# Kernel tuning notes

Hardware: AMD Instinct MI355X
Metric: run time of the kernel (lower is better)

The kernel has to match this reference:

```python
import jax, jax.numpy as jnp
import numpy as np

B, T, E, H, V = 64, 512, 512, 512, 50000

def setup_inputs() -> dict:
    key = jax.random.key(0)
    ks = jax.random.split(key, 8)
    x = jax.random.randint(ks[0], (B, T), 0, V)
    h0 = jax.random.normal(ks[1], (B, H), jnp.float32) * 0.1
    c0 = jax.random.normal(ks[2], (B, H), jnp.float32) * 0.1
    emb = jax.random.normal(ks[3], (V, E), jnp.float32) * 0.02
    emb = emb.at[0].set(0.0)  # padding_idx=0
    s_i = 1.0 / np.sqrt(H)
    W_ih = jax.random.uniform(ks[4], (4 * H, E), jnp.float32, -s_i, s_i)
    W_hh = jax.random.uniform(ks[5], (4 * H, H), jnp.float32, -s_i, s_i)
    b_ih = jax.random.uniform(ks[6], (4 * H,), jnp.float32, -s_i, s_i)
    b_hh = jax.random.uniform(ks[7], (4 * H,), jnp.float32, -s_i, s_i)
    return {"x": x, "h0": h0, "c0": c0, "emb": emb,
            "W_ih": W_ih, "W_hh": W_hh, "b_ih": b_ih, "b_hh": b_hh}

def reference(x, h0, c0, emb, W_ih, W_hh, b_ih, b_hh):
    # embedding lookup (option 'a'): [B, T, E]
    xs = emb[x]
    # precompute input-to-gate projections for all timesteps: [B, T, 4H]
    pre = jnp.einsum('bte,ge->btg', xs, W_ih) + b_ih + b_hh
    pre_t = jnp.swapaxes(pre, 0, 1)  # [T, B, 4H]

    def step(carry, p_t):
        h, c = carry
        gates = p_t + h @ W_hh.T  # [B, 4H]
        i, f, g, o = jnp.split(gates, 4, axis=-1)
        i = jax.nn.sigmoid(i)
        f = jax.nn.sigmoid(f)
        g = jnp.tanh(g)
        o = jax.nn.sigmoid(o)
        c_new = f * c + i * g
        h_new = o * jnp.tanh(c_new)
        return (h_new, c_new), h_new

    _, hs = jax.lax.scan(step, (h0, c0), pre_t)  # hs: [T, B, H]
    # original stacks per-batch lists of per-timestep hidden states -> [B, T, H]
    return jnp.swapaxes(hs, 0, 1)
```

## Files before the change

### kernel.cpp

```cpp
#include <hip/hip_runtime.h>
#include <stdint.h>

typedef __attribute__((ext_vector_type(8))) short short8;
typedef __attribute__((ext_vector_type(4))) short short4_;
typedef __attribute__((ext_vector_type(4))) float f4;
typedef __attribute__((ext_vector_type(4))) uint32_t u32x4;

#define B_ 64
#define T_ 512
#define E_ 512
#define H_ 512
#define GH 2048

static __device__ __forceinline__ uint16_t f2bf(float f) {
  uint32_t u = __builtin_bit_cast(uint32_t, f);
  uint32_t r = (u + 0x7FFFu + ((u >> 16) & 1u)) >> 16;
  return (uint16_t)r;
}
static __device__ __forceinline__ float bf2f(uint16_t b) {
  return __builtin_bit_cast(float, (uint32_t)b << 16);
}
static __device__ __forceinline__ float sigmoidf_(float x) {
  return 1.0f / (1.0f + __expf(-x));
}
static __device__ __forceinline__ float tanhf_(float x) {
  float e = __expf(-2.0f * fabsf(x));
  float t = (1.0f - e) / (1.0f + e);
  return __builtin_copysignf(t, x);
}

static __device__ __forceinline__ u32x4 ld_flag4_cc(const int* p) {
  u32x4 v;
  asm volatile("global_load_dwordx4 %0, %1, off sc0 sc1\n\ts_waitcnt vmcnt(0)"
               : "=v"(v) : "v"(p) : "memory");
  return v;
}
static __device__ __forceinline__ void ld_x4_cc(u32x4* d, const void* p) {
  asm volatile("global_load_dwordx4 %0, %1, off sc0 sc1" : "=v"(*d) : "v"(p));
}
static __device__ __forceinline__ void st_u32_cc(uint32_t* p, uint32_t v) {
  asm volatile("global_store_dword %0, %1, off sc0 sc1" :: "v"(p), "v"(v) : "memory");
}
static __device__ __forceinline__ void st_flag_cc(int* p, int v) {
  asm volatile("global_store_dword %0, %1, off sc0 sc1" :: "v"(p), "v"(v) : "memory");
}

__global__ void k_prep(const float* __restrict__ Whh, uint16_t* __restrict__ Whi_g,
                       uint16_t* __restrict__ Wlo_g) {
  int i = blockIdx.x * 256 + threadIdx.x;
  float w = Whh[i];
  uint16_t hi = f2bf(w);
  Whi_g[i] = hi;
  Wlo_g[i] = f2bf(w - bf2f(hi));
}

__global__ void k_init(const float* __restrict__ h0, uint32_t* __restrict__ hP0,
                       int* __restrict__ flags) {
  int i = blockIdx.x * 256 + threadIdx.x;
  if (i < B_ * H_) {
    float v = h0[i];
    uint16_t hi = f2bf(v);
    uint16_t lo = f2bf(v - bf2f(hi));
    hP0[i] = (uint32_t)hi | ((uint32_t)lo << 16);
  }
  if (i < 128) flags[i] = 0;
}

__launch_bounds__(256)
__global__ void k_pre(const int* __restrict__ x, const float* __restrict__ emb,
                      const float* __restrict__ Wih, const float* __restrict__ bih,
                      const float* __restrict__ bhh, float* __restrict__ pre2, int t0) {
  __shared__ uint16_t As[128 * 64];
  __shared__ uint16_t Bs[128 * 64];
  const int tid = threadIdx.x;
  const int tm = blockIdx.x >> 4;
  const int tn = blockIdx.x & 15;
  const int wid = tid >> 6, lane = tid & 63;
  const int wr = wid >> 1, wc = wid & 1;

  const int arow = tid >> 1;
  const int half = tid & 1;
  const int m = tm * 128 + arow;
  const int bb = m & 63;
  const int tt = t0 + (m >> 6);
  const int xid = x[bb * T_ + tt];
  const float* asrc = emb + (size_t)xid * E_ + half * 32;
  const float* bsrc = Wih + (size_t)(tn * 128 + arow) * E_ + half * 32;

  f4 acc[4][4];
#pragma unroll
  for (int a = 0; a < 4; ++a)
#pragma unroll
    for (int b = 0; b < 4; ++b) acc[a][b] = (f4){0.f, 0.f, 0.f, 0.f};

  for (int kk = 0; kk < 8; ++kk) {
    __syncthreads();
#pragma unroll
    for (int gi = 0; gi < 4; ++gi) {
      f4 a0 = *(const f4*)(asrc + kk * 64 + gi * 8);
      f4 a1 = *(const f4*)(asrc + kk * 64 + gi * 8 + 4);
      f4 b0 = *(const f4*)(bsrc + kk * 64 + gi * 8);
      f4 b1 = *(const f4*)(bsrc + kk * 64 + gi * 8 + 4);
      short8 va, vb;
#pragma unroll
      for (int j = 0; j < 4; ++j) {
        va[j] = (short)f2bf(a0[j]); va[4 + j] = (short)f2bf(a1[j]);
        vb[j] = (short)f2bf(b0[j]); vb[4 + j] = (short)f2bf(b1[j]);
      }
      int kq = half * 4 + gi;
      *(short8*)(As + arow * 64 + (kq ^ (arow & 7)) * 8) = va;
      *(short8*)(Bs + arow * 64 + (kq ^ (arow & 7)) * 8) = vb;
    }
    __syncthreads();
#pragma unroll
    for (int ks = 0; ks < 2; ++ks) {
      short8 af[4], bfr[4];
#pragma unroll
      for (int mi = 0; mi < 4; ++mi) {
        int row = wr * 64 + mi * 16 + (lane & 15);
        int kq = ks * 4 + (lane >> 4);
        af[mi] = *(const short8*)(As + row * 64 + (kq ^ (row & 7)) * 8);
      }
#pragma unroll
      for (int ni = 0; ni < 4; ++ni) {
        int row = wc * 64 + ni * 16 + (lane & 15);
        int kq = ks * 4 + (lane >> 4);
        bfr[ni] = *(const short8*)(Bs + row * 64 + (kq ^ (row & 7)) * 8);
      }
#pragma unroll
      for (int mi = 0; mi < 4; ++mi)
#pragma unroll
        for (int ni = 0; ni < 4; ++ni)
          acc[mi][ni] = __builtin_amdgcn_mfma_f32_16x16x32_bf16(af[mi], bfr[ni], acc[mi][ni], 0, 0, 0);
    }
  }
#pragma unroll
  for (int ni = 0; ni < 4; ++ni) {
    int n = tn * 128 + wc * 64 + ni * 16 + (lane & 15);
    float bias = bih[n] + bhh[n];
    int q = n >> 9, u = n & 511;
    int ug = u >> 4, uloc = u & 15;
    int gl = q * 16 + uloc;
#pragma unroll
    for (int mi = 0; mi < 4; ++mi) {
      int mrow = tm * 128 + wr * 64 + mi * 16 + (lane >> 4) * 4;
      int trel = mrow >> 6;
      int bbr = mrow & 63;
      f4 vst;
#pragma unroll
      for (int j = 0; j < 4; ++j) vst[j] = acc[mi][ni][j] + bias;
      float* dst = pre2 + (((size_t)trel * 32 + ug) * 4 + (bbr >> 4)) * 1024 + gl * 16 + (bbr & 15);
      __builtin_nontemporal_store(vst, (f4*)dst);
    }
  }
}

__launch_bounds__(256)
__global__ void k_lstm(const float* __restrict__ pre2, const uint16_t* __restrict__ Whi_g,
                       const uint16_t* __restrict__ Wlo_g, const float* __restrict__ c0,
                       float* __restrict__ out, uint32_t* __restrict__ hP0,
                       uint32_t* __restrict__ hP1, float* __restrict__ c_state,
                       int* __restrict__ flags, int t0, int TB) {
  extern __shared__ char smem[];
  uint16_t* WhiL = (uint16_t*)smem;
  uint16_t* WloL = (uint16_t*)(smem + 65536);
  uint16_t* Hh   = (uint16_t*)(smem + 131072);
  uint16_t* Hl   = (uint16_t*)(smem + 147456);

  const int tid = threadIdx.x;
  const int bg = blockIdx.x & 3;
  const int ug = blockIdx.x >> 2;
  const int wv = tid >> 6, lane = tid & 63;
  const int wi = lane & 15, hi4 = lane >> 4;
  const int q = wi & 3, v = wi >> 2;
  const int u = ug * 16 + wv * 4 + v;
  const int gl = q * 16 + wv * 4 + v;

  for (int it = 0; it < 16; ++it) {
    int gg = it * 256 + tid;
    int r = gg >> 6, kq = gg & 63;
    int grow = (r & 3) * 512 + ug * 16 + (r >> 4) * 4 + ((r >> 2) & 3);
    short8 whi = *(const short8*)(Whi_g + (size_t)grow * 512 + kq * 8);
    short8 wlo = *(const short8*)(Wlo_g + (size_t)grow * 512 + kq * 8);
    int kqs = (kq & ~7) | ((kq & 7) ^ (r & 7));
    *(short8*)(WhiL + r * 512 + kqs * 8) = whi;
    *(short8*)(WloL + r * 512 + kqs * 8) = wlo;
  }

  f4 c_reg;
  {
    const float* csrc = (t0 == 0) ? c0 : c_state;
    const int brow = bg * 16 + hi4 * 4;
#pragma unroll
    for (int j = 0; j < 4; ++j) c_reg[j] = csrc[(size_t)(brow + j) * H_ + u];
  }
  int* fbase = flags + bg * 32;
  int* myflag = fbase + ug;
  u32x4 fv0 = (u32x4){0, 0, 0, 0};
  float hq_prev = 0.0f;
  const int rowloc = hi4 * 4 + q;
  const int b = bg * 16 + rowloc;
  __syncthreads();

  for (int s = t0 + 1; s <= t0 + TB; ++s) {
    const uint32_t* hsrc = (((s - 1) & 1) ? hP1 : hP0) + (size_t)bg * 16 * 512;
    uint32_t* hdst = ((s & 1) ? hP1 : hP0) + (size_t)bg * 16 * 512;

    f4 accA, accB, accC;
    {
      const f4* pp = (const f4*)(pre2 + (((size_t)(s - 1 - t0) * 32 + ug) * 4 + bg) * 1024 +
                                 gl * 16 + hi4 * 4);
      accA = __builtin_nontemporal_load(pp);
      accB = (f4){0.f, 0.f, 0.f, 0.f};
      accC = accB;
    }

    {
      const int target = s - 1;
      bool ok = true;
      if (lane < 8)
        ok = (int)fv0[0] >= target && (int)fv0[1] >= target &&
             (int)fv0[2] >= target && (int)fv0[3] >= target;
      int guard = 0;
      while (!__all(ok)) {
        __builtin_amdgcn_s_sleep(1);
        ok = true;
        if (lane < 8) {
          u32x4 fv = ld_flag4_cc(fbase + lane * 4);
          ok = (int)fv[0] >= target && (int)fv[1] >= target &&
               (int)fv[2] >= target && (int)fv[3] >= target;
        }
        if (++guard > (1 << 17)) break;
      }
    }

    u32x4 d[8];
#pragma unroll
    for (int jj = 0; jj < 8; ++jj) {
      int local = jj * 64 + lane;
      int row = local >> 5;
      int u0v = wv * 128 + (local & 31) * 4;
      ld_x4_cc(&d[jj], hsrc + (size_t)row * 512 + u0v);
    }
    if (s > t0 + 1) {
      float* optr = out + (size_t)b * (T_ * H_) + (size_t)(s - 2) * H_ + u;
      asm volatile("global_store_dword %0, %1, off" :: "v"(optr), "v"(hq_prev) : "memory");
      asm volatile("s_waitcnt vmcnt(1)" ::: "memory");
    } else {
      asm volatile("s_waitcnt vmcnt(0)" ::: "memory");
    }
    __builtin_amdgcn_sched_barrier(0);
#pragma unroll
    for (int jj = 0; jj < 8; ++jj) asm volatile("" : "+v"(d[jj]));
#pragma unroll
    for (int jj = 0; jj < 8; ++jj) {
      int local = jj * 64 + lane;
      int row = local >> 5;
      int u0v = wv * 128 + (local & 31) * 4;
      int kq = u0v >> 3, half = (u0v >> 2) & 1;
      int kqs = (kq & ~7) | ((kq & 7) ^ (row & 7));
      short4_ hh, hl;
#pragma unroll
      for (int i = 0; i < 4; ++i) {
        hh[i] = (short)(d[jj][i] & 0xFFFFu);
        hl[i] = (short)(d[jj][i] >> 16);
      }
      *(short4_*)(Hh + row * 512 + kqs * 8 + half * 4) = hh;
      *(short4_*)(Hl + row * 512 + kqs * 8 + half * 4) = hl;
    }
    __syncthreads();

    f4 accA2 = (f4){0.f, 0.f, 0.f, 0.f}, accB2 = accA2, accC2 = accA2;
    const int br = wv * 16 + wi;
#pragma unroll
    for (int ks2 = 0; ks2 < 8; ++ks2) {
#pragma unroll
      for (int p = 0; p < 2; ++p) {
        int ks = ks2 * 2 + p;
        int kq = ks * 4 + hi4;
        int kqsA = (kq & ~7) | ((kq & 7) ^ (wi & 7));
        int kqsB = (kq & ~7) | ((kq & 7) ^ (br & 7));
        short8 ah = *(const short8*)(Hh + wi * 512 + kqsA * 8);
        short8 al = *(const short8*)(Hl + wi * 512 + kqsA * 8);
        short8 bh = *(const short8*)(WhiL + br * 512 + kqsB * 8);
        short8 bl = *(const short8*)(WloL + br * 512 + kqsB * 8);
        if (p == 0) {
          accA = __builtin_amdgcn_mfma_f32_16x16x32_bf16(ah, bh, accA, 0, 0, 0);
          accB = __builtin_amdgcn_mfma_f32_16x16x32_bf16(al, bh, accB, 0, 0, 0);
          accC = __builtin_amdgcn_mfma_f32_16x16x32_bf16(ah, bl, accC, 0, 0, 0);
        } else {
          accA2 = __builtin_amdgcn_mfma_f32_16x16x32_bf16(ah, bh, accA2, 0, 0, 0);
          accB2 = __builtin_amdgcn_mfma_f32_16x16x32_bf16(al, bh, accB2, 0, 0, 0);
          accC2 = __builtin_amdgcn_mfma_f32_16x16x32_bf16(ah, bl, accC2, 0, 0, 0);
        }
      }
    }

    const bool qb0 = (q & 1) != 0, qb1 = (q & 2) != 0;
    f4 a0;
#pragma unroll
    for (int j = 0; j < 4; ++j)
      a0[j] = (accA[j] + accA2[j]) + (accB[j] + accB2[j]) + (accC[j] + accC2[j]);
    f4 x1, s1a, s1b, x2a, x2b;
#pragma unroll
    for (int j = 0; j < 4; ++j) x1[j] = __shfl_xor(a0[j], 1);
#pragma unroll
    for (int j = 0; j < 4; ++j) {
      s1a[j] = qb0 ? x1[j] : a0[j];
      s1b[j] = qb0 ? a0[j] : x1[j];
    }
#pragma unroll
    for (int j = 0; j < 4; ++j) {
      x2a[j] = __shfl_xor(s1a[j], 2);
      x2b[j] = __shfl_xor(s1b[j], 2);
    }
    f4 cn, hn;
#pragma unroll
    for (int j = 0; j < 4; ++j) {
      float gi = qb1 ? x2a[j] : s1a[j];
      float gg = qb1 ? s1a[j] : x2a[j];
      float gf = qb1 ? x2b[j] : s1b[j];
      float go = qb1 ? s1b[j] : x2b[j];
      float iv = sigmoidf_(gi);
      float fv = sigmoidf_(gf);
      float gv = tanhf_(gg);
      float ov = sigmoidf_(go);
      float c2 = fv * c_reg[j] + iv * gv;
      cn[j] = c2;
      hn[j] = ov * tanhf_(c2);
    }
    c_reg = cn;
    float s01 = qb0 ? hn[1] : hn[0];
    float s23 = qb0 ? hn[3] : hn[2];
    float hq = qb1 ? s23 : s01;

    uint16_t hhi = f2bf(hq);
    uint16_t hlo = f2bf(hq - bf2f(hhi));
    st_u32_cc(hdst + (size_t)rowloc * 512 + u, (uint32_t)hhi | ((uint32_t)hlo << 16));
    if (lane < 8) ld_x4_cc(&fv0, fbase + lane * 4);
    asm volatile("s_waitcnt vmcnt(0)" ::: "memory");
    __builtin_amdgcn_sched_barrier(0);
    asm volatile("" : "+v"(fv0));
    __syncthreads();
    if (tid == 0) st_flag_cc(myflag, s);
    hq_prev = hq;
  }

  __builtin_nontemporal_store(hq_prev,
      &out[(size_t)b * (T_ * H_) + (size_t)(t0 + TB - 1) * H_ + u]);

  {
    const bool qb0 = (q & 1) != 0, qb1 = (q & 2) != 0;
    float c01 = qb0 ? c_reg[1] : c_reg[0];
    float c23 = qb0 ? c_reg[3] : c_reg[2];
    c_state[(size_t)b * H_ + u] = qb1 ? c23 : c01;
  }
}

extern "C" void kernel_launch(void* const* d_in, const int* in_sizes, int n_in,
                              void* d_out, int out_size, void* d_ws, size_t ws_size,
                              hipStream_t stream) {
  (void)in_sizes; (void)n_in; (void)out_size;
  const int* x = (const int*)d_in[0];
  const float* h0 = (const float*)d_in[1];
  const float* c0 = (const float*)d_in[2];
  const float* emb = (const float*)d_in[3];
  const float* Wih = (const float*)d_in[4];
  const float* Whh = (const float*)d_in[5];
  const float* bih = (const float*)d_in[6];
  const float* bhh = (const float*)d_in[7];
  float* out = (float*)d_out;
  char* ws = (char*)d_ws;

  int* flags = (int*)ws;
  float* c_state = (float*)(ws + 4096);
  uint32_t* hP0 = (uint32_t*)(ws + 135168);
  uint32_t* hP1 = (uint32_t*)(ws + 266240);
  uint16_t* Whi_g = (uint16_t*)(ws + 397312);
  uint16_t* Wlo_g = (uint16_t*)(ws + 2494464);
  float* pre2 = (float*)(ws + 4591616);

  int TB = 512;
  while (TB > 2 && (size_t)4591616 + (size_t)TB * 524288 > ws_size) TB >>= 1;

  (void)hipFuncSetAttribute(reinterpret_cast<const void*>(k_lstm),
                            hipFuncAttributeMaxDynamicSharedMemorySize, 163840);

  k_prep<<<dim3(4096), dim3(256), 0, stream>>>(Whh, Whi_g, Wlo_g);
  k_init<<<dim3(128), dim3(256), 0, stream>>>(h0, hP0, flags);
  for (int t0 = 0; t0 < 512; t0 += TB) {
    k_pre<<<dim3((TB * 64 / 128) * 16), dim3(256), 0, stream>>>(x, emb, Wih, bih, bhh, pre2, t0);
    k_lstm<<<dim3(128), dim3(256), 163840, stream>>>(pre2, Whi_g, Wlo_g, c0, out, hP0, hP1,
                                                     c_state, flags, t0, TB);
  }
}
```

Before: 2.268 ms.

## Fuse input projection GEMM into recurrent kernel with per-tile readiness flags

Merges the separate input-projection GEMM launch and the LSTM recurrence launch into one kernel. 128 extra blocks compute the projection tiles and publish per-tile flags, and the recurrent blocks poll those flags every 16 steps before reading pre-activations. This lets the recurrence start before the whole projection finishes, overlapping the GEMM with the sequential scan and removing a launch boundary. The cost is extra flag polling and coherent (sc0 sc1) stores and loads on the projection buffer. Each block also requests the large 160KB shared allocation, which can limit how many blocks fit per CU.

```diff
diff --git a/kernel.cpp b/kernel.cpp
--- a/kernel.cpp
+++ b/kernel.cpp
@@ -29,6 +29,12 @@
   return __builtin_copysignf(t, x);
 }
 
+static __device__ __forceinline__ int ld_flag1_cc(const int* p) {
+  int v;
+  asm volatile("global_load_dword %0, %1, off sc0 sc1\n\ts_waitcnt vmcnt(0)"
+               : "=v"(v) : "v"(p) : "memory");
+  return v;
+}
 static __device__ __forceinline__ u32x4 ld_flag4_cc(const int* p) {
   u32x4 v;
   asm volatile("global_load_dwordx4 %0, %1, off sc0 sc1\n\ts_waitcnt vmcnt(0)"
@@ -40,6 +46,9 @@
 }
 static __device__ __forceinline__ void st_u32_cc(uint32_t* p, uint32_t v) {
   asm volatile("global_store_dword %0, %1, off sc0 sc1" :: "v"(p), "v"(v) : "memory");
+}
+static __device__ __forceinline__ void st_x4_cc(void* p, u32x4 v) {
+  asm volatile("global_store_dwordx4 %0, %1, off sc0 sc1" :: "v"(p), "v"(v) : "memory");
 }
 static __device__ __forceinline__ void st_flag_cc(int* p, int v) {
   asm volatile("global_store_dword %0, %1, off sc0 sc1" :: "v"(p), "v"(v) : "memory");
@@ -63,113 +72,123 @@
     uint16_t lo = f2bf(v - bf2f(hi));
     hP0[i] = (uint32_t)hi | ((uint32_t)lo << 16);
   }
-  if (i < 128) flags[i] = 0;
+  if (i < 5120) flags[i] = 0;
 }
 
 __launch_bounds__(256)
-__global__ void k_pre(const int* __restrict__ x, const float* __restrict__ emb,
-                      const float* __restrict__ Wih, const float* __restrict__ bih,
-                      const float* __restrict__ bhh, float* __restrict__ pre2, int t0) {
-  __shared__ uint16_t As[128 * 64];
-  __shared__ uint16_t Bs[128 * 64];
+__global__ void k_fused(const int* __restrict__ x, const float* __restrict__ emb,
+                        const float* __restrict__ Wih, const float* __restrict__ bih,
+                        const float* __restrict__ bhh, const uint16_t* __restrict__ Whi_g,
+                        const uint16_t* __restrict__ Wlo_g, const float* __restrict__ c0,
+                        float* __restrict__ out, uint32_t* __restrict__ hP0,
+                        uint32_t* __restrict__ hP1, float* __restrict__ c_state,
+                        int* __restrict__ flags, float* __restrict__ pre2,
+                        int t0, int TB, int chunk1) {
+  extern __shared__ char smem[];
   const int tid = threadIdx.x;
-  const int tm = blockIdx.x >> 4;
-  const int tn = blockIdx.x & 15;
-  const int wid = tid >> 6, lane = tid & 63;
-  const int wr = wid >> 1, wc = wid & 1;
-
-  const int arow = tid >> 1;
-  const int half = tid & 1;
-  const int m = tm * 128 + arow;
-  const int bb = m & 63;
-  const int tt = t0 + (m >> 6);
-  const int xid = x[bb * T_ + tt];
-  const float* asrc = emb + (size_t)xid * E_ + half * 32;
-  const float* bsrc = Wih + (size_t)(tn * 128 + arow) * E_ + half * 32;
-
-  f4 acc[4][4];
-#pragma unroll
-  for (int a = 0; a < 4; ++a)
-#pragma unroll
-    for (int b = 0; b < 4; ++b) acc[a][b] = (f4){0.f, 0.f, 0.f, 0.f};
-
-  for (int kk = 0; kk < 8; ++kk) {
-    __syncthreads();
-#pragma unroll
-    for (int gi = 0; gi < 4; ++gi) {
-      f4 a0 = *(const f4*)(asrc + kk * 64 + gi * 8);
-      f4 a1 = *(const f4*)(asrc + kk * 64 + gi * 8 + 4);
-      f4 b0 = *(const f4*)(bsrc + kk * 64 + gi * 8);
-      f4 b1 = *(const f4*)(bsrc + kk * 64 + gi * 8 + 4);
-      short8 va, vb;
-#pragma unroll
-      for (int j = 0; j < 4; ++j) {
-        va[j] = (short)f2bf(a0[j]); va[4 + j] = (short)f2bf(a1[j]);
-        vb[j] = (short)f2bf(b0[j]); vb[4 + j] = (short)f2bf(b1[j]);
-      }
-      int kq = half * 4 + gi;
-      *(short8*)(As + arow * 64 + (kq ^ (arow & 7)) * 8) = va;
-      *(short8*)(Bs + arow * 64 + (kq ^ (arow & 7)) * 8) = vb;
-    }
-    __syncthreads();
-#pragma unroll
-    for (int ks = 0; ks < 2; ++ks) {
-      short8 af[4], bfr[4];
-#pragma unroll
-      for (int mi = 0; mi < 4; ++mi) {
-        int row = wr * 64 + mi * 16 + (lane & 15);
-        int kq = ks * 4 + (lane >> 4);
-        af[mi] = *(const short8*)(As + row * 64 + (kq ^ (row & 7)) * 8);
+  int* preflags = flags + 1024;
+
+  if (blockIdx.x < 128) {
+    uint16_t* As = (uint16_t*)smem;
+    uint16_t* Bs = (uint16_t*)(smem + 16384);
+    const int pid = blockIdx.x;
+    const int wid = tid >> 6, lane = tid & 63;
+    const int wr = wid >> 1, wc = wid & 1;
+    const int arow = tid >> 1;
+    const int half = tid & 1;
+    const int tiles_total = TB * 8;
+
+    for (int tile = pid; tile < tiles_total; tile += 128) {
+      const int tm = tile >> 4;
+      const int tn = tile & 15;
+      const int m = tm * 128 + arow;
+      const int bb = m & 63;
+      const int tt = t0 + (m >> 6);
+      const int xid = x[bb * T_ + tt];
+      const float* asrc = emb + (size_t)xid * E_ + half * 32;
+      const float* bsrc = Wih + (size_t)(tn * 128 + arow) * E_ + half * 32;
+
+      f4 acc[4][4];
+#pragma unroll
+      for (int a = 0; a < 4; ++a)
+#pragma unroll
+        for (int b = 0; b < 4; ++b) acc[a][b] = (f4){0.f, 0.f, 0.f, 0.f};
+
+      for (int kk = 0; kk < 8; ++kk) {
+        __syncthreads();
+#pragma unroll
+        for (int gi = 0; gi < 4; ++gi) {
+          f4 a0 = *(const f4*)(asrc + kk * 64 + gi * 8);
+          f4 a1 = *(const f4*)(asrc + kk * 64 + gi * 8 + 4);
+          f4 b0 = *(const f4*)(bsrc + kk * 64 + gi * 8);
+          f4 b1 = *(const f4*)(bsrc + kk * 64 + gi * 8 + 4);
+          short8 va, vb;
+#pragma unroll
+          for (int j = 0; j < 4; ++j) {
+            va[j] = (short)f2bf(a0[j]); va[4 + j] = (short)f2bf(a1[j]);
+            vb[j] = (short)f2bf(b0[j]); vb[4 + j] = (short)f2bf(b1[j]);
+          }
+          int kq = half * 4 + gi;
+          *(short8*)(As + arow * 64 + (kq ^ (arow & 7)) * 8) = va;
+          *(short8*)(Bs + arow * 64 + (kq ^ (arow & 7)) * 8) = vb;
+        }
+        __syncthreads();
+#pragma unroll
+        for (int ks = 0; ks < 2; ++ks) {
+          short8 af[4], bfr[4];
+#pragma unroll
+          for (int mi = 0; mi < 4; ++mi) {
+            int row = wr * 64 + mi * 16 + (lane & 15);
+            int kq = ks * 4 + (lane >> 4);
+            af[mi] = *(const short8*)(As + row * 64 + (kq ^ (row & 7)) * 8);
+          }
+#pragma unroll
+          for (int ni = 0; ni < 4; ++ni) {
+            int row = wc * 64 + ni * 16 + (lane & 15);
+            int kq = ks * 4 + (lane >> 4);
+            bfr[ni] = *(const short8*)(Bs + row * 64 + (kq ^ (row & 7)) * 8);
+          }
+#pragma unroll
+          for (int mi = 0; mi < 4; ++mi)
+#pragma unroll
+            for (int ni = 0; ni < 4; ++ni)
+              acc[mi][ni] = __builtin_amdgcn_mfma_f32_16x16x32_bf16(af[mi], bfr[ni], acc[mi][ni], 0, 0, 0);
+        }
       }
 #pragma unroll
       for (int ni = 0; ni < 4; ++ni) {
-        int row = wc * 64 + ni * 16 + (lane & 15);
-        int kq = ks * 4 + (lane >> 4);
-        bfr[ni] = *(const short8*)(Bs + row * 64 + (kq ^ (row & 7)) * 8);
-      }
-#pragma unroll
-      for (int mi = 0; mi < 4; ++mi)
-#pragma unroll
-        for (int ni = 0; ni < 4; ++ni)
-          acc[mi][ni] = __builtin_amdgcn_mfma_f32_16x16x32_bf16(af[mi], bfr[ni], acc[mi][ni], 0, 0, 0);
-    }
-  }
-#pragma unroll
-  for (int ni = 0; ni < 4; ++ni) {
-    int n = tn * 128 + wc * 64 + ni * 16 + (lane & 15);
-    float bias = bih[n] + bhh[n];
-    int q = n >> 9, u = n & 511;
-    int ug = u >> 4, uloc = u & 15;
-    int gl = q * 16 + uloc;
-#pragma unroll
-    for (int mi = 0; mi < 4; ++mi) {
-      int mrow = tm * 128 + wr * 64 + mi * 16 + (lane >> 4) * 4;
-      int trel = mrow >> 6;
-      int bbr = mrow & 63;
-      f4 vst;
-#pragma unroll
-      for (int j = 0; j < 4; ++j) vst[j] = acc[mi][ni][j] + bias;
-      float* dst = pre2 + (((size_t)trel * 32 + ug) * 4 + (bbr >> 4)) * 1024 + gl * 16 + (bbr & 15);
-      __builtin_nontemporal_store(vst, (f4*)dst);
-    }
-  }
-}
-
-__launch_bounds__(256)
-__global__ void k_lstm(const float* __restrict__ pre2, const uint16_t* __restrict__ Whi_g,
-                       const uint16_t* __restrict__ Wlo_g, const float* __restrict__ c0,
-                       float* __restrict__ out, uint32_t* __restrict__ hP0,
-                       uint32_t* __restrict__ hP1, float* __restrict__ c_state,
-                       int* __restrict__ flags, int t0, int TB) {
-  extern __shared__ char smem[];
+        int n = tn * 128 + wc * 64 + ni * 16 + (lane & 15);
+        float bias = bih[n] + bhh[n];
+        int q = n >> 9, u = n & 511;
+        int ug = u >> 4, uloc = u & 15;
+        int gl = q * 16 + uloc;
+#pragma unroll
+        for (int mi = 0; mi < 4; ++mi) {
+          int mrow = tm * 128 + wr * 64 + mi * 16 + (lane >> 4) * 4;
+          int trel = mrow >> 6;
+          int bbr = mrow & 63;
+          f4 vst;
+#pragma unroll
+          for (int j = 0; j < 4; ++j) vst[j] = acc[mi][ni][j] + bias;
+          float* dst = pre2 + (((size_t)trel * 32 + ug) * 4 + (bbr >> 4)) * 1024 + gl * 16 + (bbr & 15);
+          st_x4_cc(dst, __builtin_bit_cast(u32x4, vst));
+        }
+      }
+      asm volatile("s_waitcnt vmcnt(0)" ::: "memory");
+      __syncthreads();
+      if (tid == 0) st_flag_cc(preflags + tile, chunk1);
+    }
+    return;
+  }
+
   uint16_t* WhiL = (uint16_t*)smem;
   uint16_t* WloL = (uint16_t*)(smem + 65536);
   uint16_t* Hh   = (uint16_t*)(smem + 131072);
   uint16_t* Hl   = (uint16_t*)(smem + 147456);
 
-  const int tid = threadIdx.x;
-  const int bg = blockIdx.x & 3;
-  const int ug = blockIdx.x >> 2;
+  const int idx2 = blockIdx.x - 128;
+  const int bg = idx2 & 3;
+  const int ug = idx2 >> 2;
   const int wv = tid >> 6, lane = tid & 63;
   const int wi = lane & 15, hi4 = lane >> 4;
   const int q = wi & 3, v = wi >> 2;
@@ -203,16 +222,27 @@
   __syncthreads();
 
   for (int s = t0 + 1; s <= t0 + TB; ++s) {
+    const int trel = s - 1 - t0;
     const uint32_t* hsrc = (((s - 1) & 1) ? hP1 : hP0) + (size_t)bg * 16 * 512;
     uint32_t* hdst = ((s & 1) ? hP1 : hP0) + (size_t)bg * 16 * 512;
 
-    f4 accA, accB, accC;
+    if ((trel & 15) == 0) {
+      if (lane < 32) {
+        const int* fp = preflags + ((trel >> 1) + (lane >> 2)) * 16 +
+                        ((lane & 3) << 2) + (ug >> 3);
+        int guard = 0;
+        while (ld_flag1_cc(fp) < chunk1) {
+          __builtin_amdgcn_s_sleep(2);
+          if (++guard > (1 << 17)) break;
+        }
+      }
+    }
+
+    u32x4 pv;
     {
-      const f4* pp = (const f4*)(pre2 + (((size_t)(s - 1 - t0) * 32 + ug) * 4 + bg) * 1024 +
-                                 gl * 16 + hi4 * 4);
-      accA = __builtin_nontemporal_load(pp);
-      accB = (f4){0.f, 0.f, 0.f, 0.f};
-      accC = accB;
+      const float* pp = pre2 + (((size_t)trel * 32 + ug) * 4 + bg) * 1024 +
+                        gl * 16 + hi4 * 4;
+      ld_x4_cc(&pv, pp);
     }
 
     {
@@ -250,8 +280,11 @@
       asm volatile("s_waitcnt vmcnt(0)" ::: "memory");
     }
     __builtin_amdgcn_sched_barrier(0);
+    asm volatile("" : "+v"(pv));
 #pragma unroll
     for (int jj = 0; jj < 8; ++jj) asm volatile("" : "+v"(d[jj]));
+    f4 accA = __builtin_bit_cast(f4, pv);
+    f4 accB = (f4){0.f, 0.f, 0.f, 0.f}, accC = accB;
 #pragma unroll
     for (int jj = 0; jj < 8; ++jj) {
       int local = jj * 64 + lane;
@@ -373,24 +406,25 @@
   char* ws = (char*)d_ws;
 
   int* flags = (int*)ws;
-  float* c_state = (float*)(ws + 4096);
-  uint32_t* hP0 = (uint32_t*)(ws + 135168);
-  uint32_t* hP1 = (uint32_t*)(ws + 266240);
-  uint16_t* Whi_g = (uint16_t*)(ws + 397312);
-  uint16_t* Wlo_g = (uint16_t*)(ws + 2494464);
-  float* pre2 = (float*)(ws + 4591616);
+  float* c_state = (float*)(ws + 20480);
+  uint32_t* hP0 = (uint32_t*)(ws + 151552);
+  uint32_t* hP1 = (uint32_t*)(ws + 282624);
+  uint16_t* Whi_g = (uint16_t*)(ws + 413696);
+  uint16_t* Wlo_g = (uint16_t*)(ws + 2510848);
+  float* pre2 = (float*)(ws + 4608000);
 
   int TB = 512;
-  while (TB > 2 && (size_t)4591616 + (size_t)TB * 524288 > ws_size) TB >>= 1;
-
-  (void)hipFuncSetAttribute(reinterpret_cast<const void*>(k_lstm),
+  while (TB > 2 && (size_t)4608000 + (size_t)TB * 524288 > ws_size) TB >>= 1;
+
+  (void)hipFuncSetAttribute(reinterpret_cast<const void*>(k_fused),
                             hipFuncAttributeMaxDynamicSharedMemorySize, 163840);
 
   k_prep<<<dim3(4096), dim3(256), 0, stream>>>(Whh, Whi_g, Wlo_g);
   k_init<<<dim3(128), dim3(256), 0, stream>>>(h0, hP0, flags);
   for (int t0 = 0; t0 < 512; t0 += TB) {
-    k_pre<<<dim3((TB * 64 / 128) * 16), dim3(256), 0, stream>>>(x, emb, Wih, bih, bhh, pre2, t0);
-    k_lstm<<<dim3(128), dim3(256), 163840, stream>>>(pre2, Whi_g, Wlo_g, c0, out, hP0, hP1,
-                                                     c_state, flags, t0, TB);
-  }
-}
+    int chunk1 = t0 / TB + 1;
+    k_fused<<<dim3(256), dim3(256), 163840, stream>>>(x, emb, Wih, bih, bhh, Whi_g, Wlo_g,
+                                                      c0, out, hP0, hP1, c_state, flags,
+                                                      pre2, t0, TB, chunk1);
+  }
+}
```

Measured after the change: 2.102 ms. 7.4% less time.
